# Kernel optimization log

Hardware: AMD Instinct MI355X
Metric: run time of the kernel (lower is better)

The kernel has to match this reference:

```python
import jax, jax.numpy as jnp
import numpy as np

N_NODES = 100000
N_EDGES = 640000
IN_DIM = 64
HID = 128
NUM_GRAPHS = 128
MPNN_STEPS = 3
S2S_STEPS = 3


def setup_inputs() -> dict:
    key = jax.random.key(0)
    ks = jax.random.split(key, 20)
    x = jax.random.normal(ks[0], (N_NODES, IN_DIM), dtype=jnp.float32)
    edge_index = jax.random.randint(ks[1], (2, N_EDGES), 0, N_NODES, dtype=jnp.int32)
    batch = jnp.sort(jax.random.randint(ks[2], (N_NODES,), 0, NUM_GRAPHS, dtype=jnp.int32))
    s = 1.0 / np.sqrt(HID)
    params = {
        # input layer Linear(64 -> 128)
        'W_in': jax.random.normal(ks[3], (HID, IN_DIM), dtype=jnp.float32) * s,
        'b_in': jax.random.normal(ks[4], (HID,), dtype=jnp.float32) * s,
        # MGU parameters (torch.randn init in source)
        'W_f': jax.random.normal(ks[5], (HID, HID), dtype=jnp.float32),
        'U_f': jax.random.normal(ks[6], (HID, HID), dtype=jnp.float32),
        'b_f': jax.random.normal(ks[7], (HID,), dtype=jnp.float32),
        'W_h': jax.random.normal(ks[8], (HID, HID), dtype=jnp.float32),
        'U_h': jax.random.normal(ks[9], (HID, HID), dtype=jnp.float32),
        'b_h': jax.random.normal(ks[10], (HID,), dtype=jnp.float32),
        # Set2Set LSTM: input 2*HID, hidden HID, gate order i,f,g,o
        'lstm_w_ih': jax.random.normal(ks[11], (4 * HID, 2 * HID), dtype=jnp.float32) * s,
        'lstm_w_hh': jax.random.normal(ks[12], (4 * HID, HID), dtype=jnp.float32) * s,
        'lstm_b_ih': jax.random.normal(ks[13], (4 * HID,), dtype=jnp.float32) * s,
        'lstm_b_hh': jax.random.normal(ks[14], (4 * HID,), dtype=jnp.float32) * s,
        # prediction layer Linear(2*HID -> 1)
        'W_pred': jax.random.normal(ks[15], (1, 2 * HID), dtype=jnp.float32) * s,
        'b_pred': jax.random.normal(ks[16], (1,), dtype=jnp.float32) * s,
    }
    return {'x': x, 'edge_index': edge_index, 'batch': batch, **params}


def _mpnn_mgu(h, src, dst, W_f, U_f, b_f, W_h, U_h, b_h):
    # sum-aggregate neighbor messages: m_i = sum_{j->i} h_j
    m = jax.ops.segment_sum(h[src], dst, num_segments=N_NODES)  # [N, H]
    f_t = jax.nn.sigmoid(m @ W_f.T + h @ U_f.T + b_f)
    h_hat = jnp.tanh(m @ W_h.T + (f_t * h) @ U_h.T + b_h)
    return (1.0 - f_t) * h + f_t * h_hat


def _set2set(x, batch, w_ih, w_hh, b_ih, b_hh):
    G, H = NUM_GRAPHS, HID
    q_star = jnp.zeros((G, 2 * H), dtype=x.dtype)
    h_l = jnp.zeros((G, H), dtype=x.dtype)
    c_l = jnp.zeros((G, H), dtype=x.dtype)
    for _ in range(S2S_STEPS):
        gates = q_star @ w_ih.T + h_l @ w_hh.T + b_ih + b_hh  # [G, 4H]
        i, f, g, o = jnp.split(gates, 4, axis=-1)
        c_l = jax.nn.sigmoid(f) * c_l + jax.nn.sigmoid(i) * jnp.tanh(g)
        h_l = jax.nn.sigmoid(o) * jnp.tanh(c_l)
        q = h_l  # [G, H]
        # attention over nodes within each graph segment
        e = jnp.sum(x * q[batch], axis=-1)  # [N]
        e_max = jax.ops.segment_max(e, batch, num_segments=G)
        a_un = jnp.exp(e - e_max[batch])
        denom = jax.ops.segment_sum(a_un, batch, num_segments=G)
        a = a_un / denom[batch]
        r = jax.ops.segment_sum(a[:, None] * x, batch, num_segments=G)  # [G, H]
        q_star = jnp.concatenate([q, r], axis=-1)
    return q_star


def reference(x, edge_index, batch, W_in, b_in, W_f, U_f, b_f, W_h, U_h, b_h,
              lstm_w_ih, lstm_w_hh, lstm_b_ih, lstm_b_hh, W_pred, b_pred):
    h = jax.nn.relu(x @ W_in.T + b_in)  # [N, HID]
    src, dst = edge_index[0], edge_index[1]
    for _ in range(MPNN_STEPS):
        h = _mpnn_mgu(h, src, dst, W_f, U_f, b_f, W_h, U_h, b_h)
    q_star = _set2set(h, batch, lstm_w_ih, lstm_w_hh, lstm_b_ih, lstm_b_hh)  # [G, 2H]
    return q_star @ W_pred.T + b_pred  # [G, 1]
```

## Files before the change

### kernel.cpp

```cpp
#include <hip/hip_runtime.h>
#include <math.h>

#define N_NODES 100000
#define N_EDGES 640000
#define IN_DIM 64
#define HID 128
#define NGRAPH 128
#define SPLIT 4
#define PSTR 132

typedef __bf16 bf16x2 __attribute__((ext_vector_type(2)));
typedef __bf16 bf16x4 __attribute__((ext_vector_type(4)));
typedef __bf16 bf16x8 __attribute__((ext_vector_type(8)));
typedef float f32x4 __attribute__((ext_vector_type(4)));

#define LDST 136

__device__ __forceinline__ float sigmoid_f(float z) {
  return __fdividef(1.f, 1.f + __expf(-z));
}
__device__ __forceinline__ float tanh_f(float z) {
  return 1.f - __fdividef(2.f, __expf(2.f * z) + 1.f);
}

__device__ __forceinline__ void fma44(const float4 A[4], const float4 B[4], float acc[4][4]) {
#pragma unroll
  for (int i2 = 0; i2 < 4; ++i2) {
    acc[i2][0] += A[i2].x*B[0].x + A[i2].y*B[1].x + A[i2].z*B[2].x + A[i2].w*B[3].x;
    acc[i2][1] += A[i2].x*B[0].y + A[i2].y*B[1].y + A[i2].z*B[2].y + A[i2].w*B[3].y;
    acc[i2][2] += A[i2].x*B[0].z + A[i2].y*B[1].z + A[i2].z*B[2].z + A[i2].w*B[3].z;
    acc[i2][3] += A[i2].x*B[0].w + A[i2].y*B[1].w + A[i2].z*B[2].w + A[i2].w*B[3].w;
  }
}

__global__ __launch_bounds__(256) void k_input(const float* __restrict__ x,
                                               const float* __restrict__ W,
                                               const float* __restrict__ b,
                                               float* __restrict__ h) {
  __shared__ float wS[64][132];
  __shared__ float xS[32][68];
  int t = threadIdx.x;
  int nb = blockIdx.x * 32;
#pragma unroll
  for (int i = 0; i < 8; ++i) {
    int idx4 = i * 256 + t;
    int j = idx4 >> 4, kq = idx4 & 15;
    float4 v = ((const float4*)W)[j * 16 + kq];
    wS[4*kq+0][j] = v.x; wS[4*kq+1][j] = v.y; wS[4*kq+2][j] = v.z; wS[4*kq+3][j] = v.w;
  }
#pragma unroll
  for (int i = 0; i < 2; ++i) {
    int idx4 = i * 256 + t;
    int n = idx4 >> 4, kq = idx4 & 15;
    float4 v = ((const float4*)x)[(nb + n) * 16 + kq];
    *((float4*)&xS[n][4*kq]) = v;
  }
  __syncthreads();
  int bq = t & 31, a = t >> 5;
  float acc[4][4] = {};
#pragma unroll
  for (int kk4 = 0; kk4 < 16; ++kk4) {
    float4 A[4], B[4];
#pragma unroll
    for (int i2 = 0; i2 < 4; ++i2) A[i2] = *((const float4*)&xS[4*a+i2][4*kk4]);
#pragma unroll
    for (int c = 0; c < 4; ++c) B[c] = *((const float4*)&wS[4*kk4+c][4*bq]);
    fma44(A, B, acc);
  }
  float4 bb = ((const float4*)b)[bq];
  float ba[4] = {bb.x, bb.y, bb.z, bb.w};
#pragma unroll
  for (int i2 = 0; i2 < 4; ++i2) {
    float4 o;
    o.x = fmaxf(acc[i2][0] + ba[0], 0.f);
    o.y = fmaxf(acc[i2][1] + ba[1], 0.f);
    o.z = fmaxf(acc[i2][2] + ba[2], 0.f);
    o.w = fmaxf(acc[i2][3] + ba[3], 0.f);
    ((float4*)h)[(nb + 4*a + i2) * 32 + bq] = o;
  }
}

__global__ __launch_bounds__(256) void k_hist(const int* __restrict__ dst,
                                              int* __restrict__ deg) {
  int e = blockIdx.x * 256 + threadIdx.x;
  if (e < N_EDGES) atomicAdd(&deg[dst[e]], 1);
}

#define SCAN_CHUNK 4096
#define SCAN_NB 25

__global__ __launch_bounds__(256) void k_scan_part(const int* __restrict__ deg,
                                                   int* __restrict__ bsum) {
  __shared__ int red[256];
  int t = threadIdx.x, b = blockIdx.x;
  int base = b * SCAN_CHUNK + t * 16;
  int s = 0;
#pragma unroll
  for (int i = 0; i < 16; ++i) {
    int idx = base + i;
    if (idx < N_NODES) s += deg[idx];
  }
  red[t] = s;
  __syncthreads();
  for (int off = 128; off > 0; off >>= 1) {
    if (t < off) red[t] += red[t + off];
    __syncthreads();
  }
  if (t == 0) bsum[b] = red[0];
}

__global__ void k_scan_mid(const int* __restrict__ bsum, int* __restrict__ boff,
                           int* __restrict__ rowstart) {
  if (threadIdx.x == 0) {
    int run = 0;
    for (int i = 0; i < SCAN_NB; ++i) { boff[i] = run; run += bsum[i]; }
    rowstart[N_NODES] = run;
  }
}

__global__ __launch_bounds__(256) void k_scan_final(const int* __restrict__ deg,
                                                    const int* __restrict__ boff,
                                                    int* __restrict__ rowstart) {
  __shared__ int ts[256];
  int t = threadIdx.x, b = blockIdx.x;
  int base = b * SCAN_CHUNK + t * 16;
  int v[16];
  int s = 0;
#pragma unroll
  for (int i = 0; i < 16; ++i) {
    int idx = base + i;
    v[i] = (idx < N_NODES) ? deg[idx] : 0;
    s += v[i];
  }
  ts[t] = s;
  __syncthreads();
  for (int off = 1; off < 256; off <<= 1) {
    int add = (t >= off) ? ts[t - off] : 0;
    __syncthreads();
    ts[t] += add;
    __syncthreads();
  }
  int run = boff[b] + ts[t] - s;
#pragma unroll
  for (int i = 0; i < 16; ++i) {
    int idx = base + i;
    if (idx < N_NODES) rowstart[idx] = run;
    run += v[i];
  }
}

__global__ __launch_bounds__(256) void k_fill(const int* __restrict__ src,
                                              const int* __restrict__ dst,
                                              int* __restrict__ cursor,
                                              int* __restrict__ srcSorted) {
  int e = blockIdx.x * 256 + threadIdx.x;
  if (e >= N_EDGES) return;
  int d = dst[e];
  int p = atomicAdd(&cursor[d], 1);
  srcSorted[p] = src[e];
}

__global__ __launch_bounds__(256) void k_wsplit(const float* __restrict__ W0,
                                                const float* __restrict__ W1,
                                                const float* __restrict__ W2,
                                                const float* __restrict__ W3,
                                                __bf16* __restrict__ Whi,
                                                __bf16* __restrict__ Wlo) {
  int id = blockIdx.x * 256 + threadIdx.x;
  int mat = id >> 14, idx = id & 16383;
  const float* W = (mat == 0) ? W0 : (mat == 1) ? W1 : (mat == 2) ? W2 : W3;
  float v = W[idx];
  __bf16 hi = (__bf16)v;
  Whi[id] = hi;
  Wlo[id] = (__bf16)(v - (float)hi);
}

__global__ __launch_bounds__(256, 4) void k_mgu(float* __restrict__ hdst,
                                                const float* __restrict__ hsrc,
                                                const int* __restrict__ rowstart,
                                                const int* __restrict__ srcSorted,
                                                const __bf16* __restrict__ Whi,
                                                const __bf16* __restrict__ Wlo,
                                                const float* __restrict__ bfp,
                                                const float* __restrict__ bhp) {
  __shared__ __bf16 mHi[32 * LDST], mLo[32 * LDST];
  __shared__ __bf16 hHi[32 * LDST], hLo[32 * LDST];
  const int t = threadIdx.x;
  const int nb = blockIdx.x * 32;

#pragma unroll
  for (int i = 0; i < 4; ++i) {
    int idx4 = i * 256 + t;
    int n = idx4 >> 5, kq = idx4 & 31;
    float4 vh = ((const float4*)hsrc)[(nb + n) * 32 + kq];
    bf16x4 hh, hl;
    hh[0] = (__bf16)vh.x; hl[0] = (__bf16)(vh.x - (float)hh[0]);
    hh[1] = (__bf16)vh.y; hl[1] = (__bf16)(vh.y - (float)hh[1]);
    hh[2] = (__bf16)vh.z; hl[2] = (__bf16)(vh.z - (float)hh[2]);
    hh[3] = (__bf16)vh.w; hl[3] = (__bf16)(vh.w - (float)hh[3]);
    int e0 = n * LDST + 4 * kq;
    *(bf16x4*)&hHi[e0] = hh; *(bf16x4*)&hLo[e0] = hl;
  }

  {
    const int grp = t >> 5, li = t & 31;
    const float4* h4 = (const float4*)hsrc;
#pragma unroll
    for (int c = 0; c < 4; ++c) {
      int nl = c * 8 + grp;
      int node = nb + nl;
      int j0 = rowstart[node], j1 = rowstart[node + 1];
      float4 a0 = {0.f, 0.f, 0.f, 0.f}, a1 = {0.f, 0.f, 0.f, 0.f};
      float4 a2 = {0.f, 0.f, 0.f, 0.f}, a3 = {0.f, 0.f, 0.f, 0.f};
      int j = j0;
      for (; j + 3 < j1; j += 4) {
        int s0 = srcSorted[j], s1 = srcSorted[j + 1];
        int s2 = srcSorted[j + 2], s3 = srcSorted[j + 3];
        float4 v0 = h4[s0 * 32 + li];
        float4 v1 = h4[s1 * 32 + li];
        float4 v2 = h4[s2 * 32 + li];
        float4 v3 = h4[s3 * 32 + li];
        a0.x += v0.x; a0.y += v0.y; a0.z += v0.z; a0.w += v0.w;
        a1.x += v1.x; a1.y += v1.y; a1.z += v1.z; a1.w += v1.w;
        a2.x += v2.x; a2.y += v2.y; a2.z += v2.z; a2.w += v2.w;
        a3.x += v3.x; a3.y += v3.y; a3.z += v3.z; a3.w += v3.w;
      }
      if (j + 1 < j1) {
        int s0 = srcSorted[j], s1 = srcSorted[j + 1];
        float4 v0 = h4[s0 * 32 + li];
        float4 v1 = h4[s1 * 32 + li];
        a0.x += v0.x; a0.y += v0.y; a0.z += v0.z; a0.w += v0.w;
        a1.x += v1.x; a1.y += v1.y; a1.z += v1.z; a1.w += v1.w;
        j += 2;
      }
      if (j < j1) {
        int s0 = srcSorted[j];
        float4 v0 = h4[s0 * 32 + li];
        a0.x += v0.x; a0.y += v0.y; a0.z += v0.z; a0.w += v0.w;
      }
      float4 o = {a0.x + a1.x + a2.x + a3.x, a0.y + a1.y + a2.y + a3.y,
                  a0.z + a1.z + a2.z + a3.z, a0.w + a1.w + a2.w + a3.w};
      bf16x4 mh, ml;
      mh[0] = (__bf16)o.x; ml[0] = (__bf16)(o.x - (float)mh[0]);
      mh[1] = (__bf16)o.y; ml[1] = (__bf16)(o.y - (float)mh[1]);
      mh[2] = (__bf16)o.z; ml[2] = (__bf16)(o.z - (float)mh[2]);
      mh[3] = (__bf16)o.w; ml[3] = (__bf16)(o.w - (float)mh[3]);
      int e0 = nl * LDST + 4 * li;
      *(bf16x4*)&mHi[e0] = mh; *(bf16x4*)&mLo[e0] = ml;
    }
  }
  __syncthreads();

  const int w = t >> 6, l = t & 63;
  const int lj = l & 15, q = l >> 4;

  float bfj[2], bhj[2];
#pragma unroll
  for (int ct = 0; ct < 2; ++ct) {
    int j = (2 * w + ct) * 16 + lj;
    bfj[ct] = bfp[j];
    bhj[ct] = bhp[j];
  }

  f32x4 acc[2][2] = {};

#pragma unroll
  for (int kc = 0; kc < 128; kc += 32) {
    bf16x8 bwh[2], bwl[2], buh[2], bul[2];
#pragma unroll
    for (int ct = 0; ct < 2; ++ct) {
      int off = ((2 * w + ct) * 16 + lj) * 128 + kc + q * 8;
      bwh[ct] = *(const bf16x8*)&Whi[off];
      bwl[ct] = *(const bf16x8*)&Wlo[off];
      buh[ct] = *(const bf16x8*)&Whi[16384 + off];
      bul[ct] = *(const bf16x8*)&Wlo[16384 + off];
    }
#pragma unroll
    for (int rt = 0; rt < 2; ++rt) {
      int e0 = (rt * 16 + lj) * LDST + kc + q * 8;
      bf16x8 amh = *(const bf16x8*)&mHi[e0];
      bf16x8 aml = *(const bf16x8*)&mLo[e0];
      bf16x8 ahh = *(const bf16x8*)&hHi[e0];
      bf16x8 ahl = *(const bf16x8*)&hLo[e0];
#pragma unroll
      for (int ct = 0; ct < 2; ++ct) {
        f32x4 a = acc[rt][ct];
        a = __builtin_amdgcn_mfma_f32_16x16x32_bf16(amh, bwh[ct], a, 0, 0, 0);
        a = __builtin_amdgcn_mfma_f32_16x16x32_bf16(amh, bwl[ct], a, 0, 0, 0);
        a = __builtin_amdgcn_mfma_f32_16x16x32_bf16(aml, bwh[ct], a, 0, 0, 0);
        a = __builtin_amdgcn_mfma_f32_16x16x32_bf16(ahh, buh[ct], a, 0, 0, 0);
        a = __builtin_amdgcn_mfma_f32_16x16x32_bf16(ahh, bul[ct], a, 0, 0, 0);
        a = __builtin_amdgcn_mfma_f32_16x16x32_bf16(ahl, buh[ct], a, 0, 0, 0);
        acc[rt][ct] = a;
      }
    }
  }

  __syncthreads();
  float fv[2][2][4], hvv[2][2][4];
#pragma unroll
  for (int rt = 0; rt < 2; ++rt)
#pragma unroll
    for (int ct = 0; ct < 2; ++ct) {
      int j = (2 * w + ct) * 16 + lj;
#pragma unroll
      for (int r = 0; r < 4; ++r) {
        int nl = rt * 16 + q * 4 + r;
        float z = acc[rt][ct][r] + bfj[ct];
        float f = sigmoid_f(z);
        int he = nl * LDST + j;
        float hval = (float)hHi[he] + (float)hLo[he];
        float g = f * hval;
        __bf16 ghi = (__bf16)g;
        hHi[he] = ghi;
        hLo[he] = (__bf16)(g - (float)ghi);
        fv[rt][ct][r] = f;
        hvv[rt][ct][r] = hval;
        acc[rt][ct][r] = 0.f;
      }
    }
  __syncthreads();

#pragma unroll
  for (int kc = 0; kc < 128; kc += 32) {
    bf16x8 bwh[2], bwl[2], buh[2], bul[2];
#pragma unroll
    for (int ct = 0; ct < 2; ++ct) {
      int off = ((2 * w + ct) * 16 + lj) * 128 + kc + q * 8;
      bwh[ct] = *(const bf16x8*)&Whi[2 * 16384 + off];
      bwl[ct] = *(const bf16x8*)&Wlo[2 * 16384 + off];
      buh[ct] = *(const bf16x8*)&Whi[3 * 16384 + off];
      bul[ct] = *(const bf16x8*)&Wlo[3 * 16384 + off];
    }
#pragma unroll
    for (int rt = 0; rt < 2; ++rt) {
      int e0 = (rt * 16 + lj) * LDST + kc + q * 8;
      bf16x8 amh = *(const bf16x8*)&mHi[e0];
      bf16x8 aml = *(const bf16x8*)&mLo[e0];
      bf16x8 agh = *(const bf16x8*)&hHi[e0];
      bf16x8 agl = *(const bf16x8*)&hLo[e0];
#pragma unroll
      for (int ct = 0; ct < 2; ++ct) {
        f32x4 a = acc[rt][ct];
        a = __builtin_amdgcn_mfma_f32_16x16x32_bf16(amh, bwh[ct], a, 0, 0, 0);
        a = __builtin_amdgcn_mfma_f32_16x16x32_bf16(amh, bwl[ct], a, 0, 0, 0);
        a = __builtin_amdgcn_mfma_f32_16x16x32_bf16(aml, bwh[ct], a, 0, 0, 0);
        a = __builtin_amdgcn_mfma_f32_16x16x32_bf16(agh, buh[ct], a, 0, 0, 0);
        a = __builtin_amdgcn_mfma_f32_16x16x32_bf16(agh, bul[ct], a, 0, 0, 0);
        a = __builtin_amdgcn_mfma_f32_16x16x32_bf16(agl, buh[ct], a, 0, 0, 0);
        acc[rt][ct] = a;
      }
    }
  }

#pragma unroll
  for (int rt = 0; rt < 2; ++rt)
#pragma unroll
    for (int ct = 0; ct < 2; ++ct) {
      int j = (2 * w + ct) * 16 + lj;
#pragma unroll
      for (int r = 0; r < 4; ++r) {
        int node = nb + rt * 16 + q * 4 + r;
        float T = tanh_f(acc[rt][ct][r] + bhj[ct]);
        float f = fv[rt][ct][r];
        float hn = (1.f - f) * hvv[rt][ct][r] + f * T;
        hdst[node * 128 + j] = hn;
      }
    }
}

__global__ __launch_bounds__(128) void k_s2s_init(const float* __restrict__ b_ih,
                                                  const float* __restrict__ b_hh,
                                                  float* __restrict__ q_buf,
                                                  float* __restrict__ hc_buf) {
  int g = blockIdx.x, t = threadIdx.x;
  float gi = b_ih[t] + b_hh[t];
  float gf = b_ih[128 + t] + b_hh[128 + t];
  float gg = b_ih[256 + t] + b_hh[256 + t];
  float go = b_ih[384 + t] + b_hh[384 + t];
  float c = sigmoid_f(gi) * tanh_f(gg);
  float hh = sigmoid_f(go) * tanh_f(c);
  q_buf[g * 128 + t] = hh;
  hc_buf[g * 256 + t] = hh;
  hc_buf[g * 256 + 128 + t] = c;
}

__global__ __launch_bounds__(1024, 8) void k_s2s_scan(const float* __restrict__ h,
                                                      const int* __restrict__ batch,
                                                      const float* __restrict__ q_buf,
                                                      float* __restrict__ partials) {
  const int b = blockIdx.x;
  const int g = b >> 2, p = b & (SPLIT - 1);
  const int t = threadIdx.x;
  const int w = t >> 6, l = t & 63;
  const int half = l >> 5, li = l & 31;
  const int hw = 2 * w + half;
  __shared__ float redM[32], redS[32], scl[32];
  __shared__ float rPart[32][132];
  __shared__ float sMS[2];
  __shared__ int bnd[2];

  if (t < 2) {
    int tgt = g + t;
    int lo = 0, hi = N_NODES;
    while (lo < hi) { int mid = (lo + hi) >> 1; if (batch[mid] < tgt) lo = mid + 1; else hi = mid; }
    bnd[t] = lo;
  }
  __syncthreads();
  const int s0 = bnd[0], s1 = bnd[1];
  const int len = s1 - s0;
  const int ps = s0 + (len * p) / SPLIT;
  const int pe = s0 + (len * (p + 1)) / SPLIT;

  float4 qv = ((const float4*)(q_buf + g * 128))[li];
  const float q0 = qv.x, q1 = qv.y, q2 = qv.z, q3 = qv.w;

  float mw = -INFINITY, sw = 0.f;
  float4 racc = {0.f, 0.f, 0.f, 0.f};
  const float4* h4 = (const float4*)h;
  int n = ps + hw;
  for (; n + 32 < pe; n += 64) {
    float4 hv0 = h4[n * 32 + li];
    float4 hv1 = h4[(n + 32) * 32 + li];
    float v0 = hv0.x * q0 + hv0.y * q1 + hv0.z * q2 + hv0.w * q3;
    float v1 = hv1.x * q0 + hv1.y * q1 + hv1.z * q2 + hv1.w * q3;
#pragma unroll
    for (int o = 16; o > 0; o >>= 1) {
      v0 += __shfl_xor(v0, o, 64);
      v1 += __shfl_xor(v1, o, 64);
    }
    float nm = fmaxf(mw, fmaxf(v0, v1));
    float sc = __expf(mw - nm);
    float w0 = __expf(v0 - nm);
    float w1 = __expf(v1 - nm);
    sw = sw * sc + w0 + w1;
    racc.x = racc.x * sc + w0 * hv0.x + w1 * hv1.x;
    racc.y = racc.y * sc + w0 * hv0.y + w1 * hv1.y;
    racc.z = racc.z * sc + w0 * hv0.z + w1 * hv1.z;
    racc.w = racc.w * sc + w0 * hv0.w + w1 * hv1.w;
    mw = nm;
  }
  for (; n < pe; n += 32) {
    float4 hv = h4[n * 32 + li];
    float v = hv.x * q0 + hv.y * q1 + hv.z * q2 + hv.w * q3;
#pragma unroll
    for (int o = 16; o > 0; o >>= 1) v += __shfl_xor(v, o, 64);
    float nm = fmaxf(mw, v);
    float sc = __expf(mw - nm);
    float wg = __expf(v - nm);
    sw = sw * sc + wg;
    racc.x = racc.x * sc + wg * hv.x;
    racc.y = racc.y * sc + wg * hv.y;
    racc.z = racc.z * sc + wg * hv.z;
    racc.w = racc.w * sc + wg * hv.w;
    mw = nm;
  }
  if (li == 0) { redM[hw] = mw; redS[hw] = sw; }
  *(float4*)&rPart[hw][4 * li] = racc;
  __syncthreads();
  if (t == 0) {
    float M = -INFINITY;
    for (int i = 0; i < 32; ++i) M = fmaxf(M, redM[i]);
    float S = 0.f;
    for (int i = 0; i < 32; ++i) {
      float s_ = (redM[i] > -INFINITY && M > -INFINITY) ? __expf(redM[i] - M) : 0.f;
      scl[i] = s_;
      S += redS[i] * s_;
    }
    sMS[0] = M; sMS[1] = S;
  }
  __syncthreads();
  float* P = partials + (g * SPLIT + p) * PSTR;
  if (t == 0) { P[0] = sMS[0]; P[1] = sMS[1]; }
  if (t < 128) {
    float r = 0.f;
#pragma unroll
    for (int i = 0; i < 32; ++i) r += rPart[i][t] * scl[i];
    P[4 + t] = r;
  }
}

__global__ __launch_bounds__(256) void k_s2s_combine(float* __restrict__ q_buf,
                                                     float* __restrict__ hc_buf,
                                                     const float* __restrict__ partials,
                                                     const float* __restrict__ w_ih,
                                                     const float* __restrict__ w_hh,
                                                     const float* __restrict__ b_ih,
                                                     const float* __restrict__ b_hh,
                                                     const float* __restrict__ Wp,
                                                     const float* __restrict__ bp,
                                                     float* __restrict__ out,
                                                     int last) {
  const int g = blockIdx.x, t = threadIdx.x;
  __shared__ float sc[SPLIT];
  __shared__ float qstar[256];
  __shared__ float hcl[256];
  __shared__ float gates[512];
  __shared__ float invS_sh;
  const float* P = partials + g * SPLIT * PSTR;

  if (t == 0) {
    float M = -INFINITY;
#pragma unroll
    for (int p = 0; p < SPLIT; ++p) M = fmaxf(M, P[p * PSTR]);
    float S = 0.f;
#pragma unroll
    for (int p = 0; p < SPLIT; ++p) {
      float mp = P[p * PSTR];
      float s_ = (mp > -INFINITY && M > -INFINITY) ? __expf(mp - M) : 0.f;
      sc[p] = s_;
      S += P[p * PSTR + 1] * s_;
    }
    invS_sh = (S > 0.f) ? __fdividef(1.f, S) : 0.f;
  }
  if (t < 128) {
    qstar[t] = q_buf[g * 128 + t];
    hcl[t] = hc_buf[g * 256 + t];
    hcl[128 + t] = hc_buf[g * 256 + 128 + t];
  }
  __syncthreads();
  if (t < 128) {
    float r = 0.f;
#pragma unroll
    for (int p = 0; p < SPLIT; ++p) r += P[p * PSTR + 4 + t] * sc[p];
    qstar[128 + t] = r * invS_sh;
  }
  __syncthreads();

  if (last) {
    __shared__ float pr[256];
    pr[t] = qstar[t] * Wp[t];
    __syncthreads();
    if (t < 128) pr[t] += pr[t + 128];
    __syncthreads();
    if (t < 64) {
      float s = pr[t] + pr[t + 64];
#pragma unroll
      for (int o = 32; o > 0; o >>= 1) s += __shfl_xor(s, o, 64);
      if (t == 0) out[g] = s + bp[0];
    }
    return;
  }

#pragma unroll
  for (int rr = 0; rr < 2; ++rr) {
    int j = t + rr * 256;
    const float4* wi4 = (const float4*)(w_ih + j * 256);
    const float4* wh4 = (const float4*)(w_hh + j * 128);
    float s = 0.f;
#pragma unroll 8
    for (int k = 0; k < 64; ++k) {
      float4 a = wi4[k];
      float4 b = *(const float4*)&qstar[4 * k];
      s += a.x * b.x + a.y * b.y + a.z * b.z + a.w * b.w;
    }
#pragma unroll 8
    for (int k = 0; k < 32; ++k) {
      float4 a = wh4[k];
      float4 b = *(const float4*)&hcl[4 * k];
      s += a.x * b.x + a.y * b.y + a.z * b.z + a.w * b.w;
    }
    gates[j] = s + b_ih[j] + b_hh[j];
  }
  __syncthreads();
  if (t < 128) {
    float gi = gates[t], gf = gates[128 + t], gg = gates[256 + t], go = gates[384 + t];
    float c = sigmoid_f(gf) * hcl[128 + t] + sigmoid_f(gi) * tanh_f(gg);
    float hh = sigmoid_f(go) * tanh_f(c);
    hc_buf[g * 256 + t] = hh;
    hc_buf[g * 256 + 128 + t] = c;
    q_buf[g * 128 + t] = hh;
  }
}

extern "C" void kernel_launch(void* const* d_in, const int* in_sizes, int n_in,
                              void* d_out, int out_size, void* d_ws, size_t ws_size,
                              hipStream_t stream) {
  const float* x      = (const float*)d_in[0];
  const int*   ei     = (const int*)d_in[1];
  const int*   batch  = (const int*)d_in[2];
  const float* W_in   = (const float*)d_in[3];
  const float* b_in   = (const float*)d_in[4];
  const float* W_f    = (const float*)d_in[5];
  const float* U_f    = (const float*)d_in[6];
  const float* b_f    = (const float*)d_in[7];
  const float* W_h    = (const float*)d_in[8];
  const float* U_h    = (const float*)d_in[9];
  const float* b_h    = (const float*)d_in[10];
  const float* w_ih   = (const float*)d_in[11];
  const float* w_hh   = (const float*)d_in[12];
  const float* b_ih   = (const float*)d_in[13];
  const float* b_hh   = (const float*)d_in[14];
  const float* W_pred = (const float*)d_in[15];
  const float* b_pred = (const float*)d_in[16];
  float* out = (float*)d_out;

  char* ws = (char*)d_ws;
  float* h0     = (float*)(ws);
  float* h1     = (float*)(ws + 51200000);
  int*   rowstart = (int*)(ws + 103063808);
  int*   srcSorted= (int*)(ws + 103463824);
  int*   bsum   = (int*)  (ws + 106023824);
  int*   boff   = (int*)  (ws + 106023936);
  int*    deg    = (int*)(ws + 102400000);
  int*    cursor = (int*)(ws + 102400000);
  __bf16* Whi    = (__bf16*)(ws + 102400000);
  __bf16* Wlo    = (__bf16*)(ws + 102531072);
  float* q_buf    = (float*)(ws);
  float* hc_buf   = (float*)(ws + 65536);
  float* partials = (float*)(ws + 196608);

  const int* src = ei;
  const int* dst = ei + N_EDGES;

  hipMemsetAsync(deg, 0, N_NODES * 4, stream);
  k_hist<<<(N_EDGES + 255) / 256, 256, 0, stream>>>(dst, deg);
  k_scan_part<<<SCAN_NB, 256, 0, stream>>>(deg, bsum);
  k_scan_mid<<<1, 32, 0, stream>>>(bsum, boff, rowstart);
  k_scan_final<<<SCAN_NB, 256, 0, stream>>>(deg, boff, rowstart);
  hipMemcpyAsync(cursor, rowstart, N_NODES * 4, hipMemcpyDeviceToDevice, stream);
  k_fill<<<(N_EDGES + 255) / 256, 256, 0, stream>>>(src, dst, cursor, srcSorted);

  k_wsplit<<<256, 256, 0, stream>>>(W_f, U_f, W_h, U_h, Whi, Wlo);

  k_input<<<N_NODES / 32, 256, 0, stream>>>(x, W_in, b_in, h0);

  const int NBLK = N_NODES / 32;
  k_mgu<<<NBLK, 256, 0, stream>>>(h1, h0, rowstart, srcSorted, Whi, Wlo, b_f, b_h);
  k_mgu<<<NBLK, 256, 0, stream>>>(h0, h1, rowstart, srcSorted, Whi, Wlo, b_f, b_h);
  k_mgu<<<NBLK, 256, 0, stream>>>(h1, h0, rowstart, srcSorted, Whi, Wlo, b_f, b_h);

  k_s2s_init<<<NGRAPH, 128, 0, stream>>>(b_ih, b_hh, q_buf, hc_buf);
  for (int step = 0; step < 3; ++step) {
    k_s2s_scan<<<NGRAPH * SPLIT, 1024, 0, stream>>>(h1, batch, q_buf, partials);
    k_s2s_combine<<<NGRAPH, 256, 0, stream>>>(q_buf, hc_buf, partials,
                                              w_ih, w_hh, b_ih, b_hh,
                                              W_pred, b_pred, out, step == 2);
  }
}
```

Baseline: 752.9 us.

## Gather neighbor messages edge-parallel with shared-memory atomics instead of per-node loops

Replaces per-node neighbor aggregation, where each warp half walked one node's variable-length edge list, with an edge-parallel scheme over the block's whole contiguous edge range. Each edge finds its destination node by a binary search over the block's row boundaries held in shared memory, then atomically adds into an fp32 accumulator in LDS that aliases the bf16 message buffers. The aim is to balance load across degree variation and keep more gathers in flight. In exchange it adds LDS float atomics, binary-search overhead, scalar rather than float4 loads, and extra barriers and conversion passes.

```diff
diff --git a/kernel.cpp b/kernel.cpp
--- a/kernel.cpp
+++ b/kernel.cpp
@@ -183,10 +183,21 @@
                                                 const __bf16* __restrict__ Wlo,
                                                 const float* __restrict__ bfp,
                                                 const float* __restrict__ bhp) {
-  __shared__ __bf16 mHi[32 * LDST], mLo[32 * LDST];
+  __shared__ __align__(16) unsigned char mArea[32 * LDST * 2 * 2];
   __shared__ __bf16 hHi[32 * LDST], hLo[32 * LDST];
+  __shared__ int bndS[33];
+  __bf16* mHi = (__bf16*)mArea;
+  __bf16* mLo = (__bf16*)(mArea + 32 * LDST * 2);
+  float*  mAcc = (float*)mArea;
+
   const int t = threadIdx.x;
   const int nb = blockIdx.x * 32;
+
+  if (t < 33) bndS[t] = rowstart[nb + t];
+
+#pragma unroll
+  for (int i = 0; i < 4; ++i)
+    ((float4*)mAcc)[i * 256 + t] = make_float4(0.f, 0.f, 0.f, 0.f);
 
 #pragma unroll
   for (int i = 0; i < 4; ++i) {
@@ -201,53 +212,62 @@
     int e0 = n * LDST + 4 * kq;
     *(bf16x4*)&hHi[e0] = hh; *(bf16x4*)&hLo[e0] = hl;
   }
+  __syncthreads();
 
   {
-    const int grp = t >> 5, li = t & 31;
-    const float4* h4 = (const float4*)hsrc;
-#pragma unroll
-    for (int c = 0; c < 4; ++c) {
-      int nl = c * 8 + grp;
-      int node = nb + nl;
-      int j0 = rowstart[node], j1 = rowstart[node + 1];
-      float4 a0 = {0.f, 0.f, 0.f, 0.f}, a1 = {0.f, 0.f, 0.f, 0.f};
-      float4 a2 = {0.f, 0.f, 0.f, 0.f}, a3 = {0.f, 0.f, 0.f, 0.f};
-      int j = j0;
-      for (; j + 3 < j1; j += 4) {
-        int s0 = srcSorted[j], s1 = srcSorted[j + 1];
-        int s2 = srcSorted[j + 2], s3 = srcSorted[j + 3];
-        float4 v0 = h4[s0 * 32 + li];
-        float4 v1 = h4[s1 * 32 + li];
-        float4 v2 = h4[s2 * 32 + li];
-        float4 v3 = h4[s3 * 32 + li];
-        a0.x += v0.x; a0.y += v0.y; a0.z += v0.z; a0.w += v0.w;
-        a1.x += v1.x; a1.y += v1.y; a1.z += v1.z; a1.w += v1.w;
-        a2.x += v2.x; a2.y += v2.y; a2.z += v2.z; a2.w += v2.w;
-        a3.x += v3.x; a3.y += v3.y; a3.z += v3.z; a3.w += v3.w;
-      }
-      if (j + 1 < j1) {
-        int s0 = srcSorted[j], s1 = srcSorted[j + 1];
-        float4 v0 = h4[s0 * 32 + li];
-        float4 v1 = h4[s1 * 32 + li];
-        a0.x += v0.x; a0.y += v0.y; a0.z += v0.z; a0.w += v0.w;
-        a1.x += v1.x; a1.y += v1.y; a1.z += v1.z; a1.w += v1.w;
-        j += 2;
-      }
-      if (j < j1) {
-        int s0 = srcSorted[j];
-        float4 v0 = h4[s0 * 32 + li];
-        a0.x += v0.x; a0.y += v0.y; a0.z += v0.z; a0.w += v0.w;
-      }
-      float4 o = {a0.x + a1.x + a2.x + a3.x, a0.y + a1.y + a2.y + a3.y,
-                  a0.z + a1.z + a2.z + a3.z, a0.w + a1.w + a2.w + a3.w};
-      bf16x4 mh, ml;
-      mh[0] = (__bf16)o.x; ml[0] = (__bf16)(o.x - (float)mh[0]);
-      mh[1] = (__bf16)o.y; ml[1] = (__bf16)(o.y - (float)mh[1]);
-      mh[2] = (__bf16)o.z; ml[2] = (__bf16)(o.z - (float)mh[2]);
-      mh[3] = (__bf16)o.w; ml[3] = (__bf16)(o.w - (float)mh[3]);
-      int e0 = nl * LDST + 4 * li;
-      *(bf16x4*)&mHi[e0] = mh; *(bf16x4*)&mLo[e0] = ml;
-    }
+    const int li = t & 31, eg = t >> 5;
+    const int e0 = bndS[0], e1 = bndS[32];
+    int e = e0 + eg;
+    for (; e + 8 < e1; e += 16) {
+      int ea = e, eb = e + 8;
+      int sa = srcSorted[ea], sb = srcSorted[eb];
+      int loa = 0, hia = 32;
+#pragma unroll
+      for (int it = 0; it < 5; ++it) { int mid = (loa + hia) >> 1; if (bndS[mid] <= ea) loa = mid; else hia = mid; }
+      int lob = 0, hib = 32;
+#pragma unroll
+      for (int it = 0; it < 5; ++it) { int mid = (lob + hib) >> 1; if (bndS[mid] <= eb) lob = mid; else hib = mid; }
+      const float* pa = hsrc + sa * 128 + li;
+      const float* pb = hsrc + sb * 128 + li;
+      float a0 = pa[0], a1 = pa[32], a2 = pa[64], a3 = pa[96];
+      float b0 = pb[0], b1 = pb[32], b2 = pb[64], b3 = pb[96];
+      float* da = &mAcc[loa * 128 + li];
+      float* db = &mAcc[lob * 128 + li];
+      atomicAdd(da, a0); atomicAdd(da + 32, a1); atomicAdd(da + 64, a2); atomicAdd(da + 96, a3);
+      atomicAdd(db, b0); atomicAdd(db + 32, b1); atomicAdd(db + 64, b2); atomicAdd(db + 96, b3);
+    }
+    if (e < e1) {
+      int sa = srcSorted[e];
+      int loa = 0, hia = 32;
+#pragma unroll
+      for (int it = 0; it < 5; ++it) { int mid = (loa + hia) >> 1; if (bndS[mid] <= e) loa = mid; else hia = mid; }
+      const float* pa = hsrc + sa * 128 + li;
+      float a0 = pa[0], a1 = pa[32], a2 = pa[64], a3 = pa[96];
+      float* da = &mAcc[loa * 128 + li];
+      atomicAdd(da, a0); atomicAdd(da + 32, a1); atomicAdd(da + 64, a2); atomicAdd(da + 96, a3);
+    }
+  }
+  __syncthreads();
+
+  float4 cv[4];
+#pragma unroll
+  for (int i = 0; i < 4; ++i) {
+    int idx4 = i * 256 + t;
+    int n = idx4 >> 5, kq = idx4 & 31;
+    cv[i] = ((const float4*)mAcc)[n * 32 + kq];
+  }
+  __syncthreads();
+#pragma unroll
+  for (int i = 0; i < 4; ++i) {
+    int idx4 = i * 256 + t;
+    int n = idx4 >> 5, kq = idx4 & 31;
+    bf16x4 mh, ml;
+    mh[0] = (__bf16)cv[i].x; ml[0] = (__bf16)(cv[i].x - (float)mh[0]);
+    mh[1] = (__bf16)cv[i].y; ml[1] = (__bf16)(cv[i].y - (float)mh[1]);
+    mh[2] = (__bf16)cv[i].z; ml[2] = (__bf16)(cv[i].z - (float)mh[2]);
+    mh[3] = (__bf16)cv[i].w; ml[3] = (__bf16)(cv[i].w - (float)mh[3]);
+    int ee = n * LDST + 4 * kq;
+    *(bf16x4*)&mHi[ee] = mh; *(bf16x4*)&mLo[ee] = ml;
   }
   __syncthreads();
 
```

Measured after the change: 1.736 ms. 131% more time.
